# Kernel tuning notes

Measured on AMD Instinct MI355X. Metric: run time of the kernel, lower is better.

Reference implementation:

```python
import jax, jax.numpy as jnp
import numpy as np

K = 5            # SplineConv kernel_size per dim, dim=3
KC = K ** 3      # 125 weight matrices
N0, N1, N2, N3 = 32768, 8192, 2048, 512   # node counts per pooling level (8 graphs)
E0, E1, E2, E3 = 262144, 65536, 16384, 4096
B = 8
NV = B * 8       # dense 2x2x2 voxel grid per graph -> fc1 input 8*256


def spline_conv(x, edge_index, pseudo, W, root, bias):
    # degree-1 (linear) open B-spline convolution, mean aggregation,
    # plus root weight and bias (torch SplineConv defaults).
    src, dst = edge_index[0], edge_index[1]
    N, Cin = x.shape
    Kc, _, Cout = W.shape
    E = src.shape[0]
    v = pseudo * (K - 1)                               # [E,3]
    lo = jnp.clip(jnp.floor(v), 0, K - 2)
    frac = v - lo                                      # [E,3]
    lo = lo.astype(jnp.int32)
    bits = jnp.array([[(s >> d) & 1 for d in range(3)] for s in range(8)], dtype=jnp.int32)  # [8,3]
    idx = lo[:, None, :] + bits[None]                  # [E,8,3] corner grid indices
    w = jnp.where(bits[None] == 1, frac[:, None, :], 1.0 - frac[:, None, :])
    bw = jnp.prod(w, axis=-1)                          # [E,8] basis weights (sum to 1)
    kidx = idx[..., 0] + K * idx[..., 1] + K * K * idx[..., 2]  # [E,8] flat kernel index
    if N * Kc < E * Cin:
        # project every node through all 125 kernels, then gather per edge-corner
        P = jnp.einsum('nc,kco->nko', x, W)            # [N,125,Cout]
        msg = jnp.sum(bw[..., None] * P[src[:, None], kidx], axis=1)  # [E,Cout]
    else:
        # gather weight matrices per edge-corner (cheaper when Cin small)
        xs = x[src]                                    # [E,Cin]
        msg = jnp.zeros((E, Cout), x.dtype)
        for s in range(8):                             # fixed 8 corners of trilinear basis
            msg = msg + bw[:, s, None] * jnp.einsum('ec,eco->eo', xs, W[kidx[:, s]])
    agg = jax.ops.segment_sum(msg, dst, num_segments=N)
    deg = jax.ops.segment_sum(jnp.ones((E,), x.dtype), dst, num_segments=N)
    return agg / jnp.maximum(deg, 1.0)[:, None] + x @ root + bias


def pool_max(x, cluster, n_out):
    out = jax.ops.segment_max(x, cluster, num_segments=n_out)
    return jnp.where(jnp.isfinite(out), out, 0.0)      # empty voxels -> 0


def setup_inputs():
    key = jax.random.key(0)
    ks = iter(jax.random.split(key, 40))
    inp = {"x": jax.random.normal(next(ks), (N0, 1), jnp.float32)}
    levels = [(E0, N0, N1), (E1, N1, N2), (E2, N2, N3), (E3, N3, NV)]
    for l, (E, N, Nn) in enumerate(levels, start=1):
        inp[f"edge_index{l}"] = jax.random.randint(next(ks), (2, E), 0, N)
        inp[f"pseudo{l}"] = jax.random.uniform(next(ks), (E, 3), dtype=jnp.float32)
        inp[f"cluster{l}"] = jax.random.randint(next(ks), (N,), 0, Nn)
    chans = [(1, 32), (32, 64), (64, 128), (128, 256)]
    for l, (ci, co) in enumerate(chans, start=1):
        inp[f"W{l}"] = jax.random.normal(next(ks), (KC, ci, co), jnp.float32) / np.sqrt(ci * 8.0)
        inp[f"root{l}"] = jax.random.normal(next(ks), (ci, co), jnp.float32) / np.sqrt(float(ci))
        inp[f"b{l}"] = jnp.zeros((co,), jnp.float32)
    inp["fc1_w"] = jax.random.normal(next(ks), (2048, 512), jnp.float32) / np.sqrt(2048.0)
    inp["fc1_b"] = jnp.zeros((512,), jnp.float32)
    inp["fc2_w"] = jax.random.normal(next(ks), (512, 10), jnp.float32) / np.sqrt(512.0)
    inp["fc2_b"] = jnp.zeros((10,), jnp.float32)
    return inp


def reference(x, edge_index1, pseudo1, cluster1, edge_index2, pseudo2, cluster2,
              edge_index3, pseudo3, cluster3, edge_index4, pseudo4, cluster4,
              W1, root1, b1, W2, root2, b2, W3, root3, b3, W4, root4, b4,
              fc1_w, fc1_b, fc2_w, fc2_b):
    h = jax.nn.elu(spline_conv(x, edge_index1, pseudo1, W1, root1, b1))
    h = pool_max(h, cluster1, N1)                      # sparse voxel max pool 0.02
    h = jax.nn.elu(spline_conv(h, edge_index2, pseudo2, W2, root2, b2))
    h = pool_max(h, cluster2, N2)                      # sparse voxel max pool 0.04
    h = jax.nn.elu(spline_conv(h, edge_index3, pseudo3, W3, root3, b3))
    h = pool_max(h, cluster3, N3)                      # sparse voxel max pool 0.08
    h = jax.nn.elu(spline_conv(h, edge_index4, pseudo4, W4, root4, b4))
    h = pool_max(h, cluster4, NV)                      # dense 2x2x2 voxel max pool
    h = h.reshape(B, 8 * 256)
    h = jax.nn.elu(h @ fc1_w + fc1_b)                  # dropout is identity in eval mode
    return jax.nn.log_softmax(h @ fc2_w + fc2_b, axis=1)
```

## Files before the change

### kernel.cpp

```cpp
#include <hip/hip_runtime.h>

typedef __attribute__((ext_vector_type(8))) short bf16x8;
typedef __attribute__((ext_vector_type(4))) float f32x4;
typedef __attribute__((ext_vector_type(8))) unsigned short us8;

#define DEVI __device__ __forceinline__

#define MAXW2 1088
#define MAXW3 640
#define MAXW4 512


DEVI unsigned enc_pool(float f) {
  unsigned u = __float_as_uint(f);
  return (u & 0x80000000u) ? ~u : (u | 0x80000000u);
}
DEVI float dec_pool(unsigned k) {
  if (k == 0u) return 0.0f;
  return __uint_as_float((k & 0x80000000u) ? (k ^ 0x80000000u) : ~k);
}
DEVI float eluf(float x) { return x > 0.0f ? x : expm1f(x); }
DEVI unsigned short to_bf16(float f) {
  unsigned u = __float_as_uint(f);
  return (unsigned short)((u + 0x7FFFu + ((u >> 16) & 1u)) >> 16);
}

DEVI int cell_of(const float* __restrict__ ps, int e) {
  int cell = 0;
#pragma unroll
  for (int d = 0; d < 3; ++d) {
    float v = ps[e * 3 + d] * 4.0f;
    float fl = fminf(fmaxf(floorf(v), 0.0f), 3.0f);
    cell |= ((int)fl) << (2 * d);
  }
  return cell;
}

__global__ __launch_bounds__(256) void sc_convw(
    const float* __restrict__ W2, const float* __restrict__ W3, const float* __restrict__ W4,
    unsigned short* __restrict__ P2, unsigned short* __restrict__ P3, unsigned short* __restrict__ P4) {
  int u = blockIdx.x * 256 + threadIdx.x;
  const int U2 = 32000, U3 = 128000;
  const float* W; unsigned short* P; int CIN, COUT;
  if (u < U2)           { W = W2; P = P2; CIN = 32;  COUT = 64;  }
  else if (u < U2 + U3) { u -= U2; W = W3; P = P3; CIN = 64;  COUT = 128; }
  else                  { u -= U2 + U3; W = W4; P = P4; CIN = 128; COUT = 256; }
  int MAT8 = CIN * COUT / 8;
  int k = u / MAT8, off8 = u % MAT8;
  int g = off8 & 3;
  int rem = off8 >> 2;
  int n = rem % COUT, kb = rem / COUT;
  const float* ws = W + ((size_t)k * CIN + kb * 32 + g * 8) * COUT + n;
  us8 o;
#pragma unroll
  for (int j = 0; j < 8; ++j) o[j] = to_bf16(ws[(size_t)j * COUT]);
  *(us8*)(P + (size_t)u * 8) = o;
}

__global__ __launch_bounds__(256) void sc_prep(
    const int* __restrict__ ei2, const float* __restrict__ ps2,
    const int* __restrict__ ei3, const float* __restrict__ ps3,
    const int* __restrict__ ei4, const float* __restrict__ ps4,
    unsigned* __restrict__ bc2, unsigned* __restrict__ bc3, unsigned* __restrict__ bc4,
    unsigned* __restrict__ deg2, unsigned* __restrict__ deg3, unsigned* __restrict__ deg4,
    const float* __restrict__ x, const int* __restrict__ ei1, const float* __restrict__ ps1,
    const float* __restrict__ W1, float* __restrict__ agg1, unsigned* __restrict__ deg1) {
  __shared__ unsigned hist[64];
  int b = blockIdx.x, t = threadIdx.x;
  if (b < 336) {
    const int* ei; const float* ps; unsigned *bc, *deg; int E, blk, NB;
    if (b < 256)      { ei = ei2; ps = ps2; bc = bc2; deg = deg2; E = 65536; blk = b;       NB = 256; }
    else if (b < 320) { ei = ei3; ps = ps3; bc = bc3; deg = deg3; E = 16384; blk = b - 256; NB = 64;  }
    else              { ei = ei4; ps = ps4; bc = bc4; deg = deg4; E = 4096;  blk = b - 320; NB = 16;  }
    if (t < 64) hist[t] = 0;
    __syncthreads();
    int e = blk * 256 + t;
    atomicAdd(&hist[cell_of(ps, e)], 1u);
    atomicAdd(deg + ei[E + e], 1u);
    __syncthreads();
    if (t < 64) bc[(size_t)t * NB + blk] = hist[t];
    return;
  }
  b -= 336;
  int tid = b * 256 + t;
  int e = tid >> 5, o = tid & 31;
  int ebit = t & 32;
  int src = ei1[e], dst = ei1[262144 + e];
  float f[3]; int lo[3];
#pragma unroll
  for (int d = 0; d < 3; ++d) {
    float v = ps1[e * 3 + d] * 4.0f;
    float fl = fminf(fmaxf(floorf(v), 0.0f), 3.0f);
    lo[d] = (int)fl;
    f[d] = v - fl;
  }
  int so = o & 7;
  int c0 = so & 1, c1 = (so >> 1) & 1, c2 = (so >> 2) & 1;
  float bw_own = (c0 ? f[0] : 1.0f - f[0]) * (c1 ? f[1] : 1.0f - f[1]) *
                 (c2 ? f[2] : 1.0f - f[2]);
  int k_own = (lo[0] + c0) + 5 * (lo[1] + c1) + 25 * (lo[2] + c2);
  float acc = 0.f;
#pragma unroll
  for (int s = 0; s < 8; ++s) {
    float bws = __shfl(bw_own, ebit + s);
    int ks = __shfl(k_own, ebit + s);
    acc += bws * W1[ks * 32 + o];
  }
  atomicAdd(agg1 + dst * 32 + o, x[src] * acc);
  if (o == 0) atomicAdd(deg1 + dst, 1u);
}

__global__ __launch_bounds__(1024) void sc_scan_all(
    const unsigned* __restrict__ bc2, const unsigned* __restrict__ bc3,
    const unsigned* __restrict__ bc4,
    unsigned* __restrict__ bb2, unsigned* __restrict__ bb3, unsigned* __restrict__ bb4,
    unsigned* __restrict__ cnt2, unsigned* __restrict__ cnt3, unsigned* __restrict__ cnt4,
    unsigned* __restrict__ base2, unsigned* __restrict__ base3, unsigned* __restrict__ base4,
    unsigned* __restrict__ wt2, unsigned* __restrict__ wt3, unsigned* __restrict__ wt4) {
  __shared__ unsigned tot[3][64];
  __shared__ unsigned sbs[3][64];
  int t = threadIdx.x, w = t >> 6, lane = t & 63;
#pragma unroll
  for (int lvl = 0; lvl < 3; ++lvl) {
    const unsigned* bc = lvl == 0 ? bc2 : lvl == 1 ? bc3 : bc4;
    unsigned* bb = lvl == 0 ? bb2 : lvl == 1 ? bb3 : bb4;
    int NB = lvl == 0 ? 256 : lvl == 1 ? 64 : 16;
    for (int c = w; c < 64; c += 16) {
      unsigned cellsum = 0;
      for (int sub = 0; sub * 64 < NB; ++sub) {
        int bi = sub * 64 + lane;
        unsigned v = (bi < NB) ? bc[c * NB + bi] : 0u;
        int incl = (int)v;
#pragma unroll
        for (int d = 1; d < 64; d <<= 1) {
          int tv = __shfl_up(incl, d);
          if (lane >= d) incl += tv;
        }
        if (bi < NB) bb[c * NB + bi] = cellsum + (unsigned)incl - v;
        cellsum += (unsigned)__shfl(incl, 63);
      }
      if (lane == 0) tot[lvl][c] = cellsum;
    }
  }
  __syncthreads();
  if (w < 3) {
    unsigned* cnt = w == 0 ? cnt2 : w == 1 ? cnt3 : cnt4;
    unsigned* bs  = w == 0 ? base2 : w == 1 ? base3 : base4;
    unsigned* wt  = w == 0 ? wt2 : w == 1 ? wt3 : wt4;
    int NSP  = w == 0 ? 1 : w == 1 ? 2 : 4;
    int MAXW = w == 0 ? MAXW2 : w == 1 ? MAXW3 : MAXW4;
    unsigned v = tot[w][lane];
    int incl = (int)v;
#pragma unroll
    for (int d = 1; d < 64; d <<= 1) {
      int tv = __shfl_up(incl, d);
      if (lane >= d) incl += tv;
    }
    unsigned excl = (unsigned)incl - v;
    sbs[w][lane] = excl;
    cnt[lane] = v;
    bs[lane] = excl;
    int nch = (int)((v + 63) >> 6);
    int cscan = nch;
#pragma unroll
    for (int d = 1; d < 64; d <<= 1) {
      int tv = __shfl_up(cscan, d);
      if (lane >= d) cscan += tv;
    }
    int cbase = cscan - nch;
    int CT = __shfl(cscan, 63);
    for (int ch = 0; ch < nch; ++ch)
      for (int ns = 0; ns < NSP; ++ns)
        wt[(cbase + ch) * NSP + ns] = ((unsigned)lane << 16) | ((unsigned)ch << 8) | (unsigned)ns;
    for (int i = CT * NSP + lane; i < MAXW; i += 64) wt[i] = 0xFFFFFFFFu;
  }
  __syncthreads();
  for (int i = t; i < 64 * 256; i += 1024) bb2[i] += sbs[0][i >> 8];
  for (int i = t; i < 64 * 64; i += 1024)  bb3[i] += sbs[1][i >> 6];
  for (int i = t; i < 64 * 16; i += 1024)  bb4[i] += sbs[2][i >> 4];
}

__global__ __launch_bounds__(256) void sc_rank_fin1(
    const int* __restrict__ ei2, const float* __restrict__ ps2,
    const int* __restrict__ ei3, const float* __restrict__ ps3,
    const int* __restrict__ ei4, const float* __restrict__ ps4,
    const unsigned* __restrict__ bb2, const unsigned* __restrict__ bb3,
    const unsigned* __restrict__ bb4,
    int* __restrict__ eid2, int* __restrict__ eid3, int* __restrict__ eid4,
    int* __restrict__ dst2, int* __restrict__ dst3, int* __restrict__ dst4,
    const float* __restrict__ x, const float* __restrict__ agg1,
    const unsigned* __restrict__ deg1, const float* __restrict__ root1,
    const float* __restrict__ b1, const int* __restrict__ cl1,
    unsigned* __restrict__ pe1) {
  __shared__ unsigned hist[64];
  int b = blockIdx.x, t = threadIdx.x;
  if (b < 336) {
    const int* ei; const float* ps; const unsigned* bb; int *eid, *dsts; int E, blk, NB;
    if (b < 256)      { ei = ei2; ps = ps2; bb = bb2; eid = eid2; dsts = dst2; E = 65536; blk = b;       NB = 256; }
    else if (b < 320) { ei = ei3; ps = ps3; bb = bb3; eid = eid3; dsts = dst3; E = 16384; blk = b - 256; NB = 64;  }
    else              { ei = ei4; ps = ps4; bb = bb4; eid = eid4; dsts = dst4; E = 4096;  blk = b - 320; NB = 16;  }
    if (t < 64) hist[t] = 0;
    __syncthreads();
    int e = blk * 256 + t;
    int cell = cell_of(ps, e);
    unsigned r = atomicAdd(&hist[cell], 1u);
    int p = (int)(bb[cell * NB + blk] + r);
    eid[p] = e;
    dsts[p] = ei[E + e];
    return;
  }
  b -= 336;
  int tid = b * 256 + t;
  int n = tid >> 5, o = tid & 31;
  unsigned dv = deg1[n];
  float acc = agg1[tid] / (float)(dv ? dv : 1u) + b1[o] + x[n] * root1[o];
  atomicMax(pe1 + (size_t)cl1[n] * 32 + o, enc_pool(eluf(acc)));
}

template <int CIN, int COUT>
__global__ void sc_finpool(const unsigned* __restrict__ xenc, const float* __restrict__ agg,
                           const unsigned* __restrict__ deg, const float* __restrict__ root,
                           const float* __restrict__ bias, const int* __restrict__ cluster,
                           unsigned* __restrict__ pe_out, int N) {
  int tid = blockIdx.x * blockDim.x + threadIdx.x;
  if (tid >= N * COUT) return;
  int n = tid / COUT, o = tid % COUT;
  unsigned dv = deg[n];
  float acc = agg[tid] / (float)(dv ? dv : 1u) + bias[o];
#pragma unroll 4
  for (int c = 0; c < CIN; ++c)
    acc += dec_pool(xenc[n * CIN + c]) * root[c * COUT + o];
  atomicMax(pe_out + (size_t)cluster[n] * COUT + o, enc_pool(eluf(acc)));
}

template <int CIN, int COUT, int NSP>
DEVI void gemm_impl(const int* __restrict__ ei, const float* __restrict__ ps,
                    const unsigned* __restrict__ xenc, const int* __restrict__ eid,
                    const unsigned short* __restrict__ Wp,
                    const unsigned* __restrict__ cnt, const unsigned* __restrict__ base,
                    const unsigned* __restrict__ wtab, const int* __restrict__ dsts,
                    float* __restrict__ agg) {
  constexpr int K = 8 * CIN;
  constexpr int NCOL = COUT / NSP;
  constexpr int NT = NCOL / 16;
  constexpr int UPT = NCOL / 32;
  constexpr int NPASS = K / 64;
  __shared__ __attribute__((aligned(16))) unsigned char lds[2 * NCOL * 80];
  __shared__ __attribute__((aligned(16))) unsigned short ldsA[64][72];
  __shared__ float s_bw[64][8];
  __shared__ int s_src[64];
  unsigned u = wtab[blockIdx.x];
  if (u == 0xFFFFFFFFu) return;
  int cell = u >> 16, chunk = (u >> 8) & 255, nsl = u & 255;
  int n0 = nsl * NCOL;
  int m = (int)cnt[cell], cb = (int)base[cell];
  int row0 = chunk * 64;
  int tid = threadIdx.x;
  int wv = tid >> 6, lane = tid & 63, g4 = lane >> 4, ln = lane & 15;
  int lo0 = cell & 3, lo1 = (cell >> 2) & 3, lo2 = cell >> 4;
  if (tid < 64) {
    int ridx = cb + min(row0 + tid, m - 1);
    int e = eid[ridx];
    s_src[tid] = ei[e];
    float f[3];
#pragma unroll
    for (int d = 0; d < 3; ++d) {
      float v = ps[e * 3 + d] * 4.0f;
      float fl = fminf(fmaxf(floorf(v), 0.0f), 3.0f);
      f[d] = v - fl;
    }
#pragma unroll
    for (int s = 0; s < 8; ++s) {
      int b0 = s & 1, b1 = (s >> 1) & 1, b2 = (s >> 2) & 1;
      s_bw[tid][s] = (b0 ? f[0] : 1.0f - f[0]) * (b1 ? f[1] : 1.0f - f[1]) *
                     (b2 ? f[2] : 1.0f - f[2]);
    }
  }
  f32x4 acc[NT];
#pragma unroll
  for (int t = 0; t < NT; ++t) acc[t] = (f32x4){0.f, 0.f, 0.f, 0.f};
  for (int pass = 0; pass < NPASS; ++pass) {
    int k0 = pass * 64;
    __syncthreads();
#pragma unroll
    for (int i = 0; i < UPT; ++i) {
      int u16 = tid + i * 256;
      int grp = u16 / (4 * NCOL), win = u16 % (4 * NCOL);
      int kg = k0 + grp * 32;
      int s = kg / CIN, kb = (kg % CIN) >> 5;
      int b0 = s & 1, b1 = (s >> 1) & 1, b2 = (s >> 2) & 1;
      int mat = (lo0 + b0) + 5 * (lo1 + b1) + 25 * (lo2 + b2);
      const us8* srcp = (const us8*)(Wp + (size_t)mat * (CIN * COUT) +
                                     (size_t)(kb * COUT * 4 + n0 * 4 + win) * 8);
      int r = grp * NCOL + (win >> 2), gg = win & 3;
      *(us8*)(lds + r * 80 + gg * 16) = *srcp;
    }
    {
      int r = tid >> 2, q = tid & 3;
      int kg = k0 + q * 16;
      int sidx = kg / CIN;
      int c0 = kg & (CIN - 1);
      float bwv = s_bw[r][sidx];
      const uint4* xp = (const uint4*)(xenc + (size_t)s_src[r] * CIN + c0);
      uint4 xa = xp[0], xb = xp[1];
      us8 o0;
      o0[0] = to_bf16(bwv * dec_pool(xa.x)); o0[1] = to_bf16(bwv * dec_pool(xa.y));
      o0[2] = to_bf16(bwv * dec_pool(xa.z)); o0[3] = to_bf16(bwv * dec_pool(xa.w));
      o0[4] = to_bf16(bwv * dec_pool(xb.x)); o0[5] = to_bf16(bwv * dec_pool(xb.y));
      o0[6] = to_bf16(bwv * dec_pool(xb.z)); o0[7] = to_bf16(bwv * dec_pool(xb.w));
      uint4 xc = xp[2], xd = xp[3];
      us8 o1;
      o1[0] = to_bf16(bwv * dec_pool(xc.x)); o1[1] = to_bf16(bwv * dec_pool(xc.y));
      o1[2] = to_bf16(bwv * dec_pool(xc.z)); o1[3] = to_bf16(bwv * dec_pool(xc.w));
      o1[4] = to_bf16(bwv * dec_pool(xd.x)); o1[5] = to_bf16(bwv * dec_pool(xd.y));
      o1[6] = to_bf16(bwv * dec_pool(xd.z)); o1[7] = to_bf16(bwv * dec_pool(xd.w));
      *(us8*)&ldsA[r][q * 16] = o0;
      *(us8*)&ldsA[r][q * 16 + 8] = o1;
    }
    __syncthreads();
#pragma unroll
    for (int kk = 0; kk < 2; ++kk) {
      bf16x8 af = *(const bf16x8*)&ldsA[wv * 16 + ln][kk * 32 + g4 * 8];
#pragma unroll
      for (int t = 0; t < NT; ++t) {
        int r = kk * NCOL + t * 16 + ln;
        bf16x8 bfr = *(const bf16x8*)(lds + r * 80 + g4 * 16);
        acc[t] = __builtin_amdgcn_mfma_f32_16x16x32_bf16(af, bfr, acc[t], 0, 0, 0);
      }
    }
  }
  int row_b = row0 + wv * 16 + g4 * 4;
  int dstv[4];
#pragma unroll
  for (int r4 = 0; r4 < 4; ++r4)
    dstv[r4] = (row_b + r4 < m) ? dsts[cb + row_b + r4] : -1;
#pragma unroll
  for (int t = 0; t < NT; ++t) {
#pragma unroll
    for (int r4 = 0; r4 < 4; ++r4) {
      if (dstv[r4] >= 0)
        atomicAdd(agg + (size_t)dstv[r4] * COUT + n0 + t * 16 + ln, acc[t][r4]);
    }
  }
}

__global__ __launch_bounds__(256) void sc_gemm_l2(
    const int* ei, const float* ps, const unsigned* xenc, const int* eid,
    const unsigned short* Wp, const unsigned* cnt, const unsigned* base,
    const unsigned* wtab, const int* dsts, float* agg) {
  gemm_impl<32, 64, 1>(ei, ps, xenc, eid, Wp, cnt, base, wtab, dsts, agg);
}
__global__ __launch_bounds__(256) void sc_gemm_l3(
    const int* ei, const float* ps, const unsigned* xenc, const int* eid,
    const unsigned short* Wp, const unsigned* cnt, const unsigned* base,
    const unsigned* wtab, const int* dsts, float* agg) {
  gemm_impl<64, 128, 2>(ei, ps, xenc, eid, Wp, cnt, base, wtab, dsts, agg);
}
__global__ __launch_bounds__(256) void sc_gemm_l4(
    const int* ei, const float* ps, const unsigned* xenc, const int* eid,
    const unsigned short* Wp, const unsigned* cnt, const unsigned* base,
    const unsigned* wtab, const int* dsts, float* agg) {
  gemm_impl<128, 256, 4>(ei, ps, xenc, eid, Wp, cnt, base, wtab, dsts, agg);
}

__global__ void sc_fc1(const unsigned* __restrict__ xenc, const float* __restrict__ w,
                       float* __restrict__ out) {
  __shared__ float sx[8][32];
  int t = threadIdx.x;
  int j = blockIdx.x * 256 + t;
  int c0 = blockIdx.y * 32;
  {
    int b = t >> 5, c = t & 31;
    sx[b][c] = dec_pool(xenc[b * 2048 + c0 + c]);
  }
  __syncthreads();
  float acc[8];
#pragma unroll
  for (int b = 0; b < 8; ++b) acc[b] = 0.f;
#pragma unroll 4
  for (int cc = 0; cc < 32; ++cc) {
    float wv = w[(size_t)(c0 + cc) * 512 + j];
#pragma unroll
    for (int b = 0; b < 8; ++b) acc[b] += sx[b][cc] * wv;
  }
#pragma unroll
  for (int b = 0; b < 8; ++b) atomicAdd(out + b * 512 + j, acc[b]);
}

__global__ void sc_fc2(const float* __restrict__ h, const float* __restrict__ b1,
                       const float* __restrict__ w2, const float* __restrict__ b2,
                       float* __restrict__ out) {
  int b = blockIdx.x;
  int lane = threadIdx.x;
  float part[10];
#pragma unroll
  for (int o = 0; o < 10; ++o) part[o] = 0.f;
  for (int k = 0; k < 8; ++k) {
    int c = k * 64 + lane;
    float v = eluf(h[b * 512 + c] + b1[c]);
#pragma unroll
    for (int o = 0; o < 10; ++o) part[o] += v * w2[c * 10 + o];
  }
#pragma unroll
  for (int o = 0; o < 10; ++o) {
#pragma unroll
    for (int d = 32; d > 0; d >>= 1) part[o] += __shfl_down(part[o], d);
  }
  if (lane == 0) {
    float z[10], mx = -1e30f;
#pragma unroll
    for (int o = 0; o < 10; ++o) { z[o] = part[o] + b2[o]; mx = fmaxf(mx, z[o]); }
    float sum = 0.f;
#pragma unroll
    for (int o = 0; o < 10; ++o) sum += expf(z[o] - mx);
    float lse = mx + logf(sum);
#pragma unroll
    for (int o = 0; o < 10; ++o) out[b * 10 + o] = z[o] - lse;
  }
}

extern "C" void kernel_launch(void* const* d_in, const int* in_sizes, int n_in,
                              void* d_out, int out_size, void* d_ws, size_t ws_size,
                              hipStream_t stream) {
  (void)in_sizes; (void)n_in; (void)out_size; (void)ws_size;
  const float* x    = (const float*)d_in[0];
  const int*   ei1  = (const int*)d_in[1];
  const float* ps1  = (const float*)d_in[2];
  const int*   cl1  = (const int*)d_in[3];
  const int*   ei2  = (const int*)d_in[4];
  const float* ps2  = (const float*)d_in[5];
  const int*   cl2  = (const int*)d_in[6];
  const int*   ei3  = (const int*)d_in[7];
  const float* ps3  = (const float*)d_in[8];
  const int*   cl3  = (const int*)d_in[9];
  const int*   ei4  = (const int*)d_in[10];
  const float* ps4  = (const float*)d_in[11];
  const int*   cl4  = (const int*)d_in[12];
  const float* W1   = (const float*)d_in[13];
  const float* root1= (const float*)d_in[14];
  const float* b1   = (const float*)d_in[15];
  const float* W2   = (const float*)d_in[16];
  const float* root2= (const float*)d_in[17];
  const float* b2   = (const float*)d_in[18];
  const float* W3   = (const float*)d_in[19];
  const float* root3= (const float*)d_in[20];
  const float* b3   = (const float*)d_in[21];
  const float* W4   = (const float*)d_in[22];
  const float* root4= (const float*)d_in[23];
  const float* b4   = (const float*)d_in[24];
  const float* fc1w = (const float*)d_in[25];
  const float* fc1b = (const float*)d_in[26];
  const float* fc2w = (const float*)d_in[27];
  const float* fc2b = (const float*)d_in[28];
  float* out = (float*)d_out;

  char* ws = (char*)d_ws;
  size_t off = 0;
  auto alloc = [&](size_t bytes) -> void* {
    void* p = ws + off;
    off = (off + bytes + 255) & ~(size_t)255;
    return p;
  };
  float*    agg1 = (float*)alloc(32768ull * 32 * 4);
  float*    agg2 = (float*)alloc(8192ull * 64 * 4);
  float*    agg3 = (float*)alloc(2048ull * 128 * 4);
  float*    agg4 = (float*)alloc(512ull * 256 * 4);
  unsigned* deg1 = (unsigned*)alloc(32768ull * 4);
  unsigned* deg2 = (unsigned*)alloc(8192ull * 4);
  unsigned* deg3 = (unsigned*)alloc(2048ull * 4);
  unsigned* deg4 = (unsigned*)alloc(512ull * 4);
  unsigned* pe1  = (unsigned*)alloc(8192ull * 32 * 4);
  unsigned* pe2  = (unsigned*)alloc(2048ull * 64 * 4);
  unsigned* pe3  = (unsigned*)alloc(512ull * 128 * 4);
  unsigned* pe4  = (unsigned*)alloc(64ull * 256 * 4);
  float*    fc1o = (float*)alloc(8ull * 512 * 4);
  size_t zero_bytes = off;
  unsigned* bc2   = (unsigned*)alloc(64ull * 256 * 4);
  unsigned* bc3   = (unsigned*)alloc(64ull * 64 * 4);
  unsigned* bc4   = (unsigned*)alloc(64ull * 16 * 4);
  unsigned* bb2   = (unsigned*)alloc(64ull * 256 * 4);
  unsigned* bb3   = (unsigned*)alloc(64ull * 64 * 4);
  unsigned* bb4   = (unsigned*)alloc(64ull * 16 * 4);
  unsigned* cnt2  = (unsigned*)alloc(64 * 4);
  unsigned* cnt3  = (unsigned*)alloc(64 * 4);
  unsigned* cnt4  = (unsigned*)alloc(64 * 4);
  unsigned* base2 = (unsigned*)alloc(64 * 4);
  unsigned* base3 = (unsigned*)alloc(64 * 4);
  unsigned* base4 = (unsigned*)alloc(64 * 4);
  unsigned* wt2   = (unsigned*)alloc(MAXW2 * 4);
  unsigned* wt3   = (unsigned*)alloc(MAXW3 * 4);
  unsigned* wt4   = (unsigned*)alloc(MAXW4 * 4);
  int* eid2 = (int*)alloc(65536ull * 4);
  int* eid3 = (int*)alloc(16384ull * 4);
  int* eid4 = (int*)alloc(4096ull * 4);
  int* dst2 = (int*)alloc(65536ull * 4);
  int* dst3 = (int*)alloc(16384ull * 4);
  int* dst4 = (int*)alloc(4096ull * 4);
  unsigned short* Wp2 = (unsigned short*)alloc(125ull * 32 * 64 * 2);
  unsigned short* Wp3 = (unsigned short*)alloc(125ull * 64 * 128 * 2);
  unsigned short* Wp4 = (unsigned short*)alloc(125ull * 128 * 256 * 2);

  hipMemsetAsync(d_ws, 0, zero_bytes, stream);
  sc_convw<<<2625, 256, 0, stream>>>(W2, W3, W4, Wp2, Wp3, Wp4);
  sc_prep<<<33104, 256, 0, stream>>>(ei2, ps2, ei3, ps3, ei4, ps4,
                                     bc2, bc3, bc4, deg2, deg3, deg4,
                                     x, ei1, ps1, W1, agg1, deg1);
  sc_scan_all<<<1, 1024, 0, stream>>>(bc2, bc3, bc4, bb2, bb3, bb4,
                                      cnt2, cnt3, cnt4, base2, base3, base4,
                                      wt2, wt3, wt4);
  sc_rank_fin1<<<4432, 256, 0, stream>>>(ei2, ps2, ei3, ps3, ei4, ps4,
                                         bb2, bb3, bb4, eid2, eid3, eid4,
                                         dst2, dst3, dst4,
                                         x, agg1, deg1, root1, b1, cl1, pe1);

  sc_gemm_l2<<<MAXW2, 256, 0, stream>>>(ei2, ps2, pe1, eid2, Wp2, cnt2, base2, wt2, dst2, agg2);
  sc_finpool<32, 64><<<2048, 256, 0, stream>>>(pe1, agg2, deg2, root2, b2, cl2, pe2, 8192);

  sc_gemm_l3<<<MAXW3, 256, 0, stream>>>(ei3, ps3, pe2, eid3, Wp3, cnt3, base3, wt3, dst3, agg3);
  sc_finpool<64, 128><<<1024, 256, 0, stream>>>(pe2, agg3, deg3, root3, b3, cl3, pe3, 2048);

  sc_gemm_l4<<<MAXW4, 256, 0, stream>>>(ei4, ps4, pe3, eid4, Wp4, cnt4, base4, wt4, dst4, agg4);
  sc_finpool<128, 256><<<512, 256, 0, stream>>>(pe3, agg4, deg4, root4, b4, cl4, pe4, 512);

  sc_fc1<<<dim3(2, 64), 256, 0, stream>>>(pe4, fc1w, fc1o);
  sc_fc2<<<8, 64, 0, stream>>>(fc1o, fc1b, fc2w, fc2b, out);
}
```

Before: 188.3 us.

## Route layer-1 spline conv through cell-sorted MFMA path like deeper layers

Layer 1 used to be a per-edge, per-channel scalar kernel that gathered W1 for all 8 corners and issued 32 float atomics per edge. Its edges are now bucketed by spline cell with the same histogram, scan and rank pipeline as layers 2-4. A new MFMA kernel computes basis-weighted messages per 64-edge chunk, and the weight conversion is merged into the histogram kernel to save a launch. This adds a sort pass over 262K edges, extra eid/dst buffers, bf16 rounding of layer-1 messages, and an extra kernel launch for finpool1.

```diff
diff --git a/kernel.cpp b/kernel.cpp
--- a/kernel.cpp
+++ b/kernel.cpp
@@ -2,10 +2,12 @@
 
 typedef __attribute__((ext_vector_type(8))) short bf16x8;
 typedef __attribute__((ext_vector_type(4))) float f32x4;
+typedef __attribute__((ext_vector_type(4))) unsigned short us4;
 typedef __attribute__((ext_vector_type(8))) unsigned short us8;
 
 #define DEVI __device__ __forceinline__
 
+#define MAXW1 4160
 #define MAXW2 1088
 #define MAXW3 640
 #define MAXW4 512
@@ -36,95 +38,86 @@
   return cell;
 }
 
-__global__ __launch_bounds__(256) void sc_convw(
+__global__ __launch_bounds__(256) void sc_cvct(
     const float* __restrict__ W2, const float* __restrict__ W3, const float* __restrict__ W4,
-    unsigned short* __restrict__ P2, unsigned short* __restrict__ P3, unsigned short* __restrict__ P4) {
-  int u = blockIdx.x * 256 + threadIdx.x;
-  const int U2 = 32000, U3 = 128000;
-  const float* W; unsigned short* P; int CIN, COUT;
-  if (u < U2)           { W = W2; P = P2; CIN = 32;  COUT = 64;  }
-  else if (u < U2 + U3) { u -= U2; W = W3; P = P3; CIN = 64;  COUT = 128; }
-  else                  { u -= U2 + U3; W = W4; P = P4; CIN = 128; COUT = 256; }
-  int MAT8 = CIN * COUT / 8;
-  int k = u / MAT8, off8 = u % MAT8;
-  int g = off8 & 3;
-  int rem = off8 >> 2;
-  int n = rem % COUT, kb = rem / COUT;
-  const float* ws = W + ((size_t)k * CIN + kb * 32 + g * 8) * COUT + n;
-  us8 o;
-#pragma unroll
-  for (int j = 0; j < 8; ++j) o[j] = to_bf16(ws[(size_t)j * COUT]);
-  *(us8*)(P + (size_t)u * 8) = o;
-}
-
-__global__ __launch_bounds__(256) void sc_prep(
+    unsigned short* __restrict__ P2, unsigned short* __restrict__ P3, unsigned short* __restrict__ P4,
+    const int* __restrict__ ei1, const float* __restrict__ ps1,
     const int* __restrict__ ei2, const float* __restrict__ ps2,
     const int* __restrict__ ei3, const float* __restrict__ ps3,
     const int* __restrict__ ei4, const float* __restrict__ ps4,
-    unsigned* __restrict__ bc2, unsigned* __restrict__ bc3, unsigned* __restrict__ bc4,
-    unsigned* __restrict__ deg2, unsigned* __restrict__ deg3, unsigned* __restrict__ deg4,
-    const float* __restrict__ x, const int* __restrict__ ei1, const float* __restrict__ ps1,
-    const float* __restrict__ W1, float* __restrict__ agg1, unsigned* __restrict__ deg1) {
+    unsigned* __restrict__ bc1, unsigned* __restrict__ bc2,
+    unsigned* __restrict__ bc3, unsigned* __restrict__ bc4,
+    unsigned* __restrict__ deg1, unsigned* __restrict__ deg2,
+    unsigned* __restrict__ deg3, unsigned* __restrict__ deg4) {
   __shared__ unsigned hist[64];
   int b = blockIdx.x, t = threadIdx.x;
-  if (b < 336) {
+  if (b < 2625) {
+    int u = b * 256 + t;
+    const int U2 = 32000, U3 = 128000;
+    const float* W; unsigned short* P; int CIN, COUT;
+    if (u < U2)           { W = W2; P = P2; CIN = 32;  COUT = 64;  }
+    else if (u < U2 + U3) { u -= U2; W = W3; P = P3; CIN = 64;  COUT = 128; }
+    else                  { u -= U2 + U3; W = W4; P = P4; CIN = 128; COUT = 256; }
+    int MAT8 = CIN * COUT / 8;
+    int k = u / MAT8, off8 = u % MAT8;
+    int g = off8 & 3;
+    int rem = off8 >> 2;
+    int n = rem % COUT, kb = rem / COUT;
+    const float* wsrc = W + ((size_t)k * CIN + kb * 32 + g * 8) * COUT + n;
+    us8 o;
+#pragma unroll
+    for (int j = 0; j < 8; ++j) o[j] = to_bf16(wsrc[(size_t)j * COUT]);
+    *(us8*)(P + (size_t)u * 8) = o;
+    return;
+  }
+  b -= 2625;
+  if (t < 64) hist[t] = 0;
+  __syncthreads();
+  if (b < 256) {
+    int blk = b;
+#pragma unroll
+    for (int i = 0; i < 4; ++i) {
+      int e = blk * 1024 + i * 256 + t;
+      atomicAdd(&hist[cell_of(ps1, e)], 1u);
+      atomicAdd(deg1 + ei1[262144 + e], 1u);
+    }
+    __syncthreads();
+    if (t < 64) bc1[(size_t)t * 256 + blk] = hist[t];
+    return;
+  }
+  b -= 256;
+  {
     const int* ei; const float* ps; unsigned *bc, *deg; int E, blk, NB;
     if (b < 256)      { ei = ei2; ps = ps2; bc = bc2; deg = deg2; E = 65536; blk = b;       NB = 256; }
     else if (b < 320) { ei = ei3; ps = ps3; bc = bc3; deg = deg3; E = 16384; blk = b - 256; NB = 64;  }
     else              { ei = ei4; ps = ps4; bc = bc4; deg = deg4; E = 4096;  blk = b - 320; NB = 16;  }
-    if (t < 64) hist[t] = 0;
-    __syncthreads();
     int e = blk * 256 + t;
     atomicAdd(&hist[cell_of(ps, e)], 1u);
     atomicAdd(deg + ei[E + e], 1u);
     __syncthreads();
     if (t < 64) bc[(size_t)t * NB + blk] = hist[t];
-    return;
-  }
-  b -= 336;
-  int tid = b * 256 + t;
-  int e = tid >> 5, o = tid & 31;
-  int ebit = t & 32;
-  int src = ei1[e], dst = ei1[262144 + e];
-  float f[3]; int lo[3];
-#pragma unroll
-  for (int d = 0; d < 3; ++d) {
-    float v = ps1[e * 3 + d] * 4.0f;
-    float fl = fminf(fmaxf(floorf(v), 0.0f), 3.0f);
-    lo[d] = (int)fl;
-    f[d] = v - fl;
-  }
-  int so = o & 7;
-  int c0 = so & 1, c1 = (so >> 1) & 1, c2 = (so >> 2) & 1;
-  float bw_own = (c0 ? f[0] : 1.0f - f[0]) * (c1 ? f[1] : 1.0f - f[1]) *
-                 (c2 ? f[2] : 1.0f - f[2]);
-  int k_own = (lo[0] + c0) + 5 * (lo[1] + c1) + 25 * (lo[2] + c2);
-  float acc = 0.f;
-#pragma unroll
-  for (int s = 0; s < 8; ++s) {
-    float bws = __shfl(bw_own, ebit + s);
-    int ks = __shfl(k_own, ebit + s);
-    acc += bws * W1[ks * 32 + o];
-  }
-  atomicAdd(agg1 + dst * 32 + o, x[src] * acc);
-  if (o == 0) atomicAdd(deg1 + dst, 1u);
+  }
 }
 
 __global__ __launch_bounds__(1024) void sc_scan_all(
-    const unsigned* __restrict__ bc2, const unsigned* __restrict__ bc3,
-    const unsigned* __restrict__ bc4,
-    unsigned* __restrict__ bb2, unsigned* __restrict__ bb3, unsigned* __restrict__ bb4,
-    unsigned* __restrict__ cnt2, unsigned* __restrict__ cnt3, unsigned* __restrict__ cnt4,
-    unsigned* __restrict__ base2, unsigned* __restrict__ base3, unsigned* __restrict__ base4,
-    unsigned* __restrict__ wt2, unsigned* __restrict__ wt3, unsigned* __restrict__ wt4) {
-  __shared__ unsigned tot[3][64];
-  __shared__ unsigned sbs[3][64];
+    const unsigned* __restrict__ bc1, const unsigned* __restrict__ bc2,
+    const unsigned* __restrict__ bc3, const unsigned* __restrict__ bc4,
+    unsigned* __restrict__ bb1, unsigned* __restrict__ bb2,
+    unsigned* __restrict__ bb3, unsigned* __restrict__ bb4,
+    unsigned* __restrict__ cnt1, unsigned* __restrict__ cnt2,
+    unsigned* __restrict__ cnt3, unsigned* __restrict__ cnt4,
+    unsigned* __restrict__ base1, unsigned* __restrict__ base2,
+    unsigned* __restrict__ base3, unsigned* __restrict__ base4,
+    unsigned* __restrict__ wt1, unsigned* __restrict__ wt2,
+    unsigned* __restrict__ wt3, unsigned* __restrict__ wt4) {
+  __shared__ unsigned tot[4][64];
+  __shared__ unsigned sbs[4][64];
   int t = threadIdx.x, w = t >> 6, lane = t & 63;
 #pragma unroll
-  for (int lvl = 0; lvl < 3; ++lvl) {
-    const unsigned* bc = lvl == 0 ? bc2 : lvl == 1 ? bc3 : bc4;
-    unsigned* bb = lvl == 0 ? bb2 : lvl == 1 ? bb3 : bb4;
-    int NB = lvl == 0 ? 256 : lvl == 1 ? 64 : 16;
+  for (int lvl = 0; lvl < 4; ++lvl) {
+    const unsigned* bc = lvl == 0 ? bc1 : lvl == 1 ? bc2 : lvl == 2 ? bc3 : bc4;
+    unsigned* bb = lvl == 0 ? bb1 : lvl == 1 ? bb2 : lvl == 2 ? bb3 : bb4;
+    int NB = lvl <= 1 ? 256 : lvl == 2 ? 64 : 16;
     for (int c = w; c < 64; c += 16) {
       unsigned cellsum = 0;
       for (int sub = 0; sub * 64 < NB; ++sub) {
@@ -143,12 +136,12 @@
     }
   }
   __syncthreads();
-  if (w < 3) {
-    unsigned* cnt = w == 0 ? cnt2 : w == 1 ? cnt3 : cnt4;
-    unsigned* bs  = w == 0 ? base2 : w == 1 ? base3 : base4;
-    unsigned* wt  = w == 0 ? wt2 : w == 1 ? wt3 : wt4;
-    int NSP  = w == 0 ? 1 : w == 1 ? 2 : 4;
-    int MAXW = w == 0 ? MAXW2 : w == 1 ? MAXW3 : MAXW4;
+  if (w < 4) {
+    unsigned* cnt = w == 0 ? cnt1 : w == 1 ? cnt2 : w == 2 ? cnt3 : cnt4;
+    unsigned* bs  = w == 0 ? base1 : w == 1 ? base2 : w == 2 ? base3 : base4;
+    unsigned* wt  = w == 0 ? wt1 : w == 1 ? wt2 : w == 2 ? wt3 : wt4;
+    int NSP  = w <= 1 ? 1 : w == 2 ? 2 : 4;
+    int MAXW = w == 0 ? MAXW1 : w == 1 ? MAXW2 : w == 2 ? MAXW3 : MAXW4;
     unsigned v = tot[w][lane];
     int incl = (int)v;
 #pragma unroll
@@ -175,42 +168,138 @@
     for (int i = CT * NSP + lane; i < MAXW; i += 64) wt[i] = 0xFFFFFFFFu;
   }
   __syncthreads();
-  for (int i = t; i < 64 * 256; i += 1024) bb2[i] += sbs[0][i >> 8];
-  for (int i = t; i < 64 * 64; i += 1024)  bb3[i] += sbs[1][i >> 6];
-  for (int i = t; i < 64 * 16; i += 1024)  bb4[i] += sbs[2][i >> 4];
-}
-
-__global__ __launch_bounds__(256) void sc_rank_fin1(
+  for (int i = t; i < 64 * 256; i += 1024) bb1[i] += sbs[0][i >> 8];
+  for (int i = t; i < 64 * 256; i += 1024) bb2[i] += sbs[1][i >> 8];
+  for (int i = t; i < 64 * 64; i += 1024)  bb3[i] += sbs[2][i >> 6];
+  for (int i = t; i < 64 * 16; i += 1024)  bb4[i] += sbs[3][i >> 4];
+}
+
+__global__ __launch_bounds__(256) void sc_rank_all(
+    const int* __restrict__ ei1, const float* __restrict__ ps1,
     const int* __restrict__ ei2, const float* __restrict__ ps2,
     const int* __restrict__ ei3, const float* __restrict__ ps3,
     const int* __restrict__ ei4, const float* __restrict__ ps4,
-    const unsigned* __restrict__ bb2, const unsigned* __restrict__ bb3,
-    const unsigned* __restrict__ bb4,
-    int* __restrict__ eid2, int* __restrict__ eid3, int* __restrict__ eid4,
-    int* __restrict__ dst2, int* __restrict__ dst3, int* __restrict__ dst4,
-    const float* __restrict__ x, const float* __restrict__ agg1,
-    const unsigned* __restrict__ deg1, const float* __restrict__ root1,
-    const float* __restrict__ b1, const int* __restrict__ cl1,
-    unsigned* __restrict__ pe1) {
+    const unsigned* __restrict__ bb1, const unsigned* __restrict__ bb2,
+    const unsigned* __restrict__ bb3, const unsigned* __restrict__ bb4,
+    int* __restrict__ eid1, int* __restrict__ eid2, int* __restrict__ eid3,
+    int* __restrict__ eid4,
+    int* __restrict__ dst1, int* __restrict__ dst2, int* __restrict__ dst3,
+    int* __restrict__ dst4) {
   __shared__ unsigned hist[64];
   int b = blockIdx.x, t = threadIdx.x;
-  if (b < 336) {
-    const int* ei; const float* ps; const unsigned* bb; int *eid, *dsts; int E, blk, NB;
-    if (b < 256)      { ei = ei2; ps = ps2; bb = bb2; eid = eid2; dsts = dst2; E = 65536; blk = b;       NB = 256; }
-    else if (b < 320) { ei = ei3; ps = ps3; bb = bb3; eid = eid3; dsts = dst3; E = 16384; blk = b - 256; NB = 64;  }
-    else              { ei = ei4; ps = ps4; bb = bb4; eid = eid4; dsts = dst4; E = 4096;  blk = b - 320; NB = 16;  }
-    if (t < 64) hist[t] = 0;
-    __syncthreads();
-    int e = blk * 256 + t;
-    int cell = cell_of(ps, e);
-    unsigned r = atomicAdd(&hist[cell], 1u);
-    int p = (int)(bb[cell * NB + blk] + r);
-    eid[p] = e;
-    dsts[p] = ei[E + e];
+  if (t < 64) hist[t] = 0;
+  __syncthreads();
+  if (b < 256) {
+    int blk = b;
+#pragma unroll
+    for (int i = 0; i < 4; ++i) {
+      int e = blk * 1024 + i * 256 + t;
+      int cell = cell_of(ps1, e);
+      unsigned r = atomicAdd(&hist[cell], 1u);
+      int p = (int)(bb1[cell * 256 + blk] + r);
+      eid1[p] = e;
+      dst1[p] = ei1[262144 + e];
+    }
     return;
   }
-  b -= 336;
-  int tid = b * 256 + t;
+  b -= 256;
+  const int* ei; const float* ps; const unsigned* bb; int *eid, *dsts; int E, blk, NB;
+  if (b < 256)      { ei = ei2; ps = ps2; bb = bb2; eid = eid2; dsts = dst2; E = 65536; blk = b;       NB = 256; }
+  else if (b < 320) { ei = ei3; ps = ps3; bb = bb3; eid = eid3; dsts = dst3; E = 16384; blk = b - 256; NB = 64;  }
+  else              { ei = ei4; ps = ps4; bb = bb4; eid = eid4; dsts = dst4; E = 4096;  blk = b - 320; NB = 16;  }
+  int e = blk * 256 + t;
+  int cell = cell_of(ps, e);
+  unsigned r = atomicAdd(&hist[cell], 1u);
+  int p = (int)(bb[cell * NB + blk] + r);
+  eid[p] = e;
+  dsts[p] = ei[E + e];
+}
+
+__global__ __launch_bounds__(256) void sc_gemm_l1(
+    const int* __restrict__ ei, const float* __restrict__ ps,
+    const float* __restrict__ x, const int* __restrict__ eid,
+    const float* __restrict__ W1, const unsigned* __restrict__ cnt,
+    const unsigned* __restrict__ base, const unsigned* __restrict__ wtab,
+    const int* __restrict__ dsts, float* __restrict__ agg) {
+  __shared__ __attribute__((aligned(16))) unsigned short ldsA[64][40];
+  __shared__ __attribute__((aligned(16))) unsigned short ldsB[32][40];
+  unsigned u = wtab[blockIdx.x];
+  if (u == 0xFFFFFFFFu) return;
+  int cell = u >> 16, chunk = (u >> 8) & 255;
+  int m = (int)cnt[cell], cb = (int)base[cell];
+  int row0 = chunk * 64;
+  int tid = threadIdx.x;
+  int wv = tid >> 6, lane = tid & 63, g4 = lane >> 4, ln = lane & 15;
+  int lo0 = cell & 3, lo1 = (cell >> 2) & 3, lo2 = cell >> 4;
+  if (tid < 64) {
+    int ridx = cb + min(row0 + tid, m - 1);
+    int e = eid[ridx];
+    float xv = x[ei[e]];
+    float f[3];
+#pragma unroll
+    for (int d = 0; d < 3; ++d) {
+      float v = ps[e * 3 + d] * 4.0f;
+      float fl = fminf(fmaxf(floorf(v), 0.0f), 3.0f);
+      f[d] = v - fl;
+    }
+    us8 a0;
+#pragma unroll
+    for (int s = 0; s < 8; ++s) {
+      int b0 = s & 1, b1 = (s >> 1) & 1, b2 = s >> 2;
+      float bw = (b0 ? f[0] : 1.0f - f[0]) * (b1 ? f[1] : 1.0f - f[1]) *
+                 (b2 ? f[2] : 1.0f - f[2]);
+      a0[s] = to_bf16(bw * xv);
+    }
+    us8 z = {0, 0, 0, 0, 0, 0, 0, 0};
+    *(us8*)&ldsA[tid][0] = a0;
+    *(us8*)&ldsA[tid][8] = z;
+    *(us8*)&ldsA[tid][16] = z;
+    *(us8*)&ldsA[tid][24] = z;
+  }
+  {
+    int n2 = tid >> 3, kq = tid & 7;
+    us4 bv;
+#pragma unroll
+    for (int j = 0; j < 4; ++j) {
+      int k = kq * 4 + j;
+      if (k < 8) {
+        int b0 = k & 1, b1 = (k >> 1) & 1, b2 = k >> 2;
+        int mat = (lo0 + b0) + 5 * (lo1 + b1) + 25 * (lo2 + b2);
+        bv[j] = to_bf16(W1[mat * 32 + n2]);
+      } else bv[j] = 0;
+    }
+    *(us4*)&ldsB[n2][kq * 4] = bv;
+  }
+  __syncthreads();
+  f32x4 acc[2];
+  acc[0] = (f32x4){0.f, 0.f, 0.f, 0.f};
+  acc[1] = (f32x4){0.f, 0.f, 0.f, 0.f};
+  bf16x8 af = *(const bf16x8*)&ldsA[wv * 16 + ln][g4 * 8];
+#pragma unroll
+  for (int t = 0; t < 2; ++t) {
+    bf16x8 bfr = *(const bf16x8*)&ldsB[t * 16 + ln][g4 * 8];
+    acc[t] = __builtin_amdgcn_mfma_f32_16x16x32_bf16(af, bfr, acc[t], 0, 0, 0);
+  }
+  int row_b = row0 + wv * 16 + g4 * 4;
+  int dstv[4];
+#pragma unroll
+  for (int r4 = 0; r4 < 4; ++r4)
+    dstv[r4] = (row_b + r4 < m) ? dsts[cb + row_b + r4] : -1;
+#pragma unroll
+  for (int t = 0; t < 2; ++t) {
+#pragma unroll
+    for (int r4 = 0; r4 < 4; ++r4) {
+      if (dstv[r4] >= 0)
+        atomicAdd(agg + (size_t)dstv[r4] * 32 + t * 16 + ln, acc[t][r4]);
+    }
+  }
+}
+
+__global__ void sc_finpool1(const float* __restrict__ x, const float* __restrict__ agg1,
+                            const unsigned* __restrict__ deg1, const float* __restrict__ root1,
+                            const float* __restrict__ b1, const int* __restrict__ cl1,
+                            unsigned* __restrict__ pe1) {
+  int tid = blockIdx.x * 256 + threadIdx.x;
   int n = tid >> 5, o = tid & 31;
   unsigned dv = deg1[n];
   float acc = agg1[tid] / (float)(dv ? dv : 1u) + b1[o] + x[n] * root1[o];
@@ -475,24 +564,31 @@
   unsigned* pe4  = (unsigned*)alloc(64ull * 256 * 4);
   float*    fc1o = (float*)alloc(8ull * 512 * 4);
   size_t zero_bytes = off;
+  unsigned* bc1   = (unsigned*)alloc(64ull * 256 * 4);
   unsigned* bc2   = (unsigned*)alloc(64ull * 256 * 4);
   unsigned* bc3   = (unsigned*)alloc(64ull * 64 * 4);
   unsigned* bc4   = (unsigned*)alloc(64ull * 16 * 4);
+  unsigned* bb1   = (unsigned*)alloc(64ull * 256 * 4);
   unsigned* bb2   = (unsigned*)alloc(64ull * 256 * 4);
   unsigned* bb3   = (unsigned*)alloc(64ull * 64 * 4);
   unsigned* bb4   = (unsigned*)alloc(64ull * 16 * 4);
+  unsigned* cnt1  = (unsigned*)alloc(64 * 4);
   unsigned* cnt2  = (unsigned*)alloc(64 * 4);
   unsigned* cnt3  = (unsigned*)alloc(64 * 4);
   unsigned* cnt4  = (unsigned*)alloc(64 * 4);
+  unsigned* base1 = (unsigned*)alloc(64 * 4);
   unsigned* base2 = (unsigned*)alloc(64 * 4);
   unsigned* base3 = (unsigned*)alloc(64 * 4);
   unsigned* base4 = (unsigned*)alloc(64 * 4);
+  unsigned* wt1   = (unsigned*)alloc(MAXW1 * 4);
   unsigned* wt2   = (unsigned*)alloc(MAXW2 * 4);
   unsigned* wt3   = (unsigned*)alloc(MAXW3 * 4);
   unsigned* wt4   = (unsigned*)alloc(MAXW4 * 4);
+  int* eid1 = (int*)alloc(262144ull * 4);
   int* eid2 = (int*)alloc(65536ull * 4);
   int* eid3 = (int*)alloc(16384ull * 4);
   int* eid4 = (int*)alloc(4096ull * 4);
+  int* dst1 = (int*)alloc(262144ull * 4);
   int* dst2 = (int*)alloc(65536ull * 4);
   int* dst3 = (int*)alloc(16384ull * 4);
   int* dst4 = (int*)alloc(4096ull * 4);
@@ -501,17 +597,20 @@
   unsigned short* Wp4 = (unsigned short*)alloc(125ull * 128 * 256 * 2);
 
   hipMemsetAsync(d_ws, 0, zero_bytes, stream);
-  sc_convw<<<2625, 256, 0, stream>>>(W2, W3, W4, Wp2, Wp3, Wp4);
-  sc_prep<<<33104, 256, 0, stream>>>(ei2, ps2, ei3, ps3, ei4, ps4,
-                                     bc2, bc3, bc4, deg2, deg3, deg4,
-                                     x, ei1, ps1, W1, agg1, deg1);
-  sc_scan_all<<<1, 1024, 0, stream>>>(bc2, bc3, bc4, bb2, bb3, bb4,
-                                      cnt2, cnt3, cnt4, base2, base3, base4,
-                                      wt2, wt3, wt4);
-  sc_rank_fin1<<<4432, 256, 0, stream>>>(ei2, ps2, ei3, ps3, ei4, ps4,
-                                         bb2, bb3, bb4, eid2, eid3, eid4,
-                                         dst2, dst3, dst4,
-                                         x, agg1, deg1, root1, b1, cl1, pe1);
+  sc_cvct<<<3217, 256, 0, stream>>>(W2, W3, W4, Wp2, Wp3, Wp4,
+                                    ei1, ps1, ei2, ps2, ei3, ps3, ei4, ps4,
+                                    bc1, bc2, bc3, bc4, deg1, deg2, deg3, deg4);
+  sc_scan_all<<<1, 1024, 0, stream>>>(bc1, bc2, bc3, bc4, bb1, bb2, bb3, bb4,
+                                      cnt1, cnt2, cnt3, cnt4,
+                                      base1, base2, base3, base4,
+                                      wt1, wt2, wt3, wt4);
+  sc_rank_all<<<592, 256, 0, stream>>>(ei1, ps1, ei2, ps2, ei3, ps3, ei4, ps4,
+                                       bb1, bb2, bb3, bb4,
+                                       eid1, eid2, eid3, eid4,
+                                       dst1, dst2, dst3, dst4);
+
+  sc_gemm_l1<<<MAXW1, 256, 0, stream>>>(ei1, ps1, x, eid1, W1, cnt1, base1, wt1, dst1, agg1);
+  sc_finpool1<<<4096, 256, 0, stream>>>(x, agg1, deg1, root1, b1, cl1, pe1);
 
   sc_gemm_l2<<<MAXW2, 256, 0, stream>>>(ei2, ps2, pe1, eid2, Wp2, cnt2, base2, wt2, dst2, agg2);
   sc_finpool<32, 64><<<2048, 256, 0, stream>>>(pe1, agg2, deg2, root2, b2, cl2, pe2, 8192);
```

After: 209.3 us. 11.1% more time.
